# Kernel optimization log

Hardware: AMD Instinct MI355X
Metric: run time of the kernel (lower is better)

## Reference

```python
import jax, jax.numpy as jnp
import numpy as np

B, S, D = 8, 2048, 512

def setup_inputs() -> dict:
    key = jax.random.key(0)
    k1, k2 = jax.random.split(key)
    lstm_out = jax.random.normal(k1, (B, S, D), dtype=jnp.float32)
    # xavier_uniform init for [D, D]
    limit = float(np.sqrt(6.0 / (D + D)))
    attention_weights = jax.random.uniform(k2, (D, D), dtype=jnp.float32, minval=-limit, maxval=limit)
    return {"lstm_out": lstm_out, "attention_weights": attention_weights}

def reference(lstm_out, attention_weights):
    # scores[b,i,j] = tanh( (x W) x^T )
    proj = jnp.einsum('bsd,de->bse', lstm_out, attention_weights)          # [B,S,D]
    scores = jnp.tanh(jnp.einsum('bsd,btd->bst', proj, lstm_out))          # [B,S,S]
    attn = jax.nn.softmax(scores, axis=-1)                                 # [B,S,S]
    return jnp.einsum('bst,btd->bsd', attn, lstm_out)                      # [B,S,D]
```

## Files before the change

### kernel.cpp

```cpp
#include <hip/hip_runtime.h>
#include <hip/hip_bf16.h>

typedef __bf16 bf16;
typedef __attribute__((ext_vector_type(4))) __bf16 bf16x4;
typedef __attribute__((ext_vector_type(8))) __bf16 bf16x8;
typedef __attribute__((ext_vector_type(4))) float floatx4;

#define NSLOT 32

__device__ __forceinline__ void gl_lds16(const bf16* g, bf16* l) {
    __builtin_amdgcn_global_load_lds(
        (const __attribute__((address_space(1))) unsigned int*)g,
        (__attribute__((address_space(3))) unsigned int*)l,
        16, 0, 0);
}

__device__ __forceinline__ void swizzle_mn(int& bm, int& bn) {
    int gx = gridDim.x;
    int f  = blockIdx.y * gx + blockIdx.x;
    int st = f >> 3, r = f & 7;
    int mgroups = gx >> 2;
    bm = (st % mgroups) * 4 + (r & 3);
    bn = (st / mgroups) * 2 + (r >> 2);
}

__global__ __launch_bounds__(256) void cast_both(const float* __restrict__ in,
                                                 bf16* __restrict__ outn,
                                                 bf16* __restrict__ outt,
                                                 int R, int C) {
    __shared__ float tile[64][65];
    const long long bz = blockIdx.z;
    in   += bz * (long long)R * C;
    outn += bz * (long long)R * C;
    outt += bz * (long long)R * C;
    const int r0 = blockIdx.x * 64, c0 = blockIdx.y * 64;
    const int cl = (threadIdx.x & 15) * 4;
    const int rw = threadIdx.x >> 4;
#pragma unroll
    for (int it = 0; it < 4; ++it) {
        const int r = rw + it * 16;
        floatx4 v = *(const floatx4*)&in[(long long)(r0 + r) * C + c0 + cl];
        bf16x4 b; b[0] = (bf16)v[0]; b[1] = (bf16)v[1]; b[2] = (bf16)v[2]; b[3] = (bf16)v[3];
        *(bf16x4*)&outn[(long long)(r0 + r) * C + c0 + cl] = b;
        tile[r][cl + 0] = v[0]; tile[r][cl + 1] = v[1];
        tile[r][cl + 2] = v[2]; tile[r][cl + 3] = v[3];
    }
    __syncthreads();
#pragma unroll
    for (int it = 0; it < 4; ++it) {
        const int c = rw + it * 16;
        bf16x4 b;
        b[0] = (bf16)tile[cl + 0][c]; b[1] = (bf16)tile[cl + 1][c];
        b[2] = (bf16)tile[cl + 2][c]; b[3] = (bf16)tile[cl + 3][c];
        *(bf16x4*)&outt[(long long)(c0 + c) * R + r0 + cl] = b;
    }
}

__global__ __launch_bounds__(256) void cast_transpose(const float* __restrict__ in,
                                                      bf16* __restrict__ out,
                                                      int R, int C) {
    __shared__ float tile[32][33];
    const int r0 = blockIdx.x * 32, c0 = blockIdx.y * 32;
    const int tx = threadIdx.x & 31, ty = threadIdx.x >> 5;
#pragma unroll
    for (int i = 0; i < 32; i += 8)
        tile[ty + i][tx] = in[(long long)(r0 + ty + i) * C + (c0 + tx)];
    __syncthreads();
#pragma unroll
    for (int i = 0; i < 32; i += 8)
        out[(long long)(c0 + ty + i) * R + (r0 + tx)] = (bf16)tile[tx][ty + i];
}

__device__ __forceinline__ float fast_tanh(float v) {
    float e = __expf(2.0f * v);
    return 1.0f - 2.0f / (e + 1.0f);
}

template <int MODE>
__global__ __launch_bounds__(256) void gemm128(const bf16* __restrict__ A,
                                               const bf16* __restrict__ Bm,
                                               void* __restrict__ Cout,
                                               float* __restrict__ rpart,
                                               int M, int N, int K,
                                               long long batchA, long long batchB,
                                               long long batchC, long long batchR) {
    const long long bz = blockIdx.z;
    A  += bz * batchA;
    Bm += bz * batchB;

    __shared__ bf16 As[2][128 * 32];
    __shared__ bf16 Bs[2][128 * 32];
    __shared__ float rs[128];

    const int t    = threadIdx.x;
    const int lane = t & 63;
    const int wave = t >> 6;
    const int quad = lane >> 4;
    const int l16  = lane & 15;

    int bm, bn;
    swizzle_mn(bm, bn);
    const int m0 = bm * 128;
    const int n0 = bn * 128;
    const int wm = (wave >> 1) * 64;
    const int wn = (wave & 1) * 64;

    floatx4 acc[4][4] = {};

    const int srow = t >> 2;
    const int sch  = (((t & 3) ^ ((t >> 3) & 3))) * 8;
    const bf16* Abase = A + (long long)(m0 + srow) * K + sch;
    const bf16* Bbase = Bm + (long long)(n0 + srow) * K + sch;
    const long long r64 = 64LL * K;

    const int rdch = (quad ^ ((l16 >> 1) & 3)) * 8;

    if (MODE == 2) {
        if (t < 128) {
            const float* pp = rpart + (bz * batchR + m0 + t) * NSLOT;
            float s = 0.f;
#pragma unroll
            for (int c = 0; c < NSLOT / 4; ++c) {
                float4 p = ((const float4*)pp)[c];
                s += (p.x + p.y) + (p.z + p.w);
            }
            rs[t] = 1.0f / s;
        }
    }

    auto stage = [&](int buf, int k0) {
        gl_lds16(Abase + k0,       &As[buf][t * 8]);
        gl_lds16(Abase + k0 + r64, &As[buf][t * 8 + 2048]);
        gl_lds16(Bbase + k0,       &Bs[buf][t * 8]);
        gl_lds16(Bbase + k0 + r64, &Bs[buf][t * 8 + 2048]);
    };

    auto compute = [&](int buf) {
        bf16x8 af[4], bfr[4];
#pragma unroll
        for (int i = 0; i < 4; ++i)
            af[i] = *(const bf16x8*)(&As[buf][(wm + i * 16 + l16) * 32 + rdch]);
#pragma unroll
        for (int j = 0; j < 4; ++j)
            bfr[j] = *(const bf16x8*)(&Bs[buf][(wn + j * 16 + l16) * 32 + rdch]);
#pragma unroll
        for (int i = 0; i < 4; ++i)
#pragma unroll
            for (int j = 0; j < 4; ++j)
                acc[i][j] = __builtin_amdgcn_mfma_f32_16x16x32_bf16(af[i], bfr[j], acc[i][j], 0, 0, 0);
    };

    const int NT  = K >> 5;
    const int f   = blockIdx.y * gridDim.x + blockIdx.x;
    const int off = (f & 3) * (NT >> 2);

    stage(0, ((0 + off) & (NT - 1)) << 5);
    __syncthreads();
    for (int it = 0; it < NT; ++it) {
        const int buf = it & 1;
        if (it + 1 < NT) stage(buf ^ 1, ((it + 1 + off) & (NT - 1)) << 5);
        compute(buf);
        __syncthreads();
    }

    if (MODE == 1) {
        bf16* Cg = (bf16*)Cout + bz * batchC;
        const int slot = bn * 2 + (wave & 1);
#pragma unroll
        for (int i = 0; i < 4; ++i)
#pragma unroll
            for (int r = 0; r < 4; ++r) {
                long long row = m0 + wm + i * 16 + quad * 4 + r;
                float s = 0.f;
#pragma unroll
                for (int j = 0; j < 4; ++j) {
                    float v = __expf(fast_tanh(acc[i][j][r]));
                    s += v;
                    Cg[row * (long long)N + (n0 + wn + j * 16 + l16)] = (bf16)v;
                }
#pragma unroll
                for (int msk = 1; msk < 16; msk <<= 1) s += __shfl_xor(s, msk);
                if (l16 == 0)
                    rpart[(bz * batchR + row) * NSLOT + slot] = s;
            }
    } else if (MODE == 2) {
        float* Og = (float*)Cout + bz * batchC;
#pragma unroll
        for (int i = 0; i < 4; ++i)
#pragma unroll
            for (int r = 0; r < 4; ++r) {
                int rl = wm + i * 16 + quad * 4 + r;
                float inv = rs[rl];
                long long row = m0 + rl;
#pragma unroll
                for (int j = 0; j < 4; ++j)
                    Og[row * (long long)N + (n0 + wn + j * 16 + l16)] = acc[i][j][r] * inv;
            }
    } else {
        bf16* Cg = (bf16*)Cout + bz * batchC;
#pragma unroll
        for (int i = 0; i < 4; ++i)
#pragma unroll
            for (int r = 0; r < 4; ++r) {
                long long row = m0 + wm + i * 16 + quad * 4 + r;
#pragma unroll
                for (int j = 0; j < 4; ++j)
                    Cg[row * (long long)N + (n0 + wn + j * 16 + l16)] = (bf16)acc[i][j][r];
            }
    }
}

extern "C" void kernel_launch(void* const* d_in, const int* in_sizes, int n_in,
                              void* d_out, int out_size, void* d_ws, size_t ws_size,
                              hipStream_t stream) {
    const int B = 8, S = 2048, D = 512;
    const float* x = (const float*)d_in[0];
    const float* W = (const float*)d_in[1];
    float* out = (float*)d_out;

    const size_t nx = (size_t)B * S * D;
    const size_t nw = (size_t)D * D;

    char* ws = (char*)d_ws;
    auto al = [](size_t v) { return (v + 255) & ~(size_t)255; };
    size_t off = 0;
    bf16* xb = (bf16*)(ws + off); off = al(off + nx * 2);
    bf16* xt = (bf16*)(ws + off); off = al(off + nx * 2);
    bf16* pb = (bf16*)(ws + off); off = al(off + nx * 2);
    bf16* wt = (bf16*)(ws + off); off = al(off + nw * 2);
    float* rpart = (float*)(ws + off); off = al(off + (size_t)B * S * NSLOT * 4);
    bf16* sb = (bf16*)(ws + off);
    const size_t full_need = off + (size_t)B * S * S * 2;
    const bool batched = (ws_size >= full_need);

    { dim3 g(S / 64, D / 64, B); cast_both<<<g, 256, 0, stream>>>(x, xb, xt, S, D); }
    { dim3 g(D / 32, D / 32, 1); cast_transpose<<<g, 256, 0, stream>>>(W, wt, D, D); }

    {
        dim3 g(B * S / 128, D / 128, 1);
        gemm128<0><<<g, 256, 0, stream>>>(xb, wt, (void*)pb, nullptr, B * S, D, D, 0, 0, 0, 0);
    }

    const long long sd = (long long)S * D;
    const long long ss = (long long)S * S;

    if (batched) {
        dim3 g2(S / 128, S / 128, B);
        gemm128<1><<<g2, 256, 0, stream>>>(pb, xb, (void*)sb, rpart, S, S, D, sd, sd, ss, S);
        dim3 g4(S / 128, D / 128, B);
        gemm128<2><<<g4, 256, 0, stream>>>(sb, xt, (void*)out, rpart, S, D, S, ss, sd, sd, S);
    } else {
        for (int b = 0; b < B; ++b) {
            dim3 g2(S / 128, S / 128, 1);
            gemm128<1><<<g2, 256, 0, stream>>>(pb + (size_t)b * sd, xb + (size_t)b * sd,
                                               (void*)sb, rpart + (size_t)b * S * NSLOT,
                                               S, S, D, 0, 0, 0, S);
            dim3 g4(S / 128, D / 128, 1);
            gemm128<2><<<g4, 256, 0, stream>>>(sb, xt + (size_t)b * sd,
                                               (void*)(out + (size_t)b * sd), rpart + (size_t)b * S * NSLOT,
                                               S, D, S, 0, 0, 0, S);
        }
    }
}
```

Measured before the change: 218.2 us.

## Enlarge GEMM block tile to 256x128 with 512 threads and drop K stagger

Doubles the M dimension of each GEMM block tile to 256 rows using eight waves per block, so each staged B tile is shared by twice as many rows. This cuts global/L2 traffic for the B operand and halves the number of blocks. The per-block rotated K start offset is removed, so all blocks now walk K from zero. This may increase L2 channel contention, and the larger LDS footprint may reduce occupancy.

Result: slower. 223.3 us (+2.3%).

```diff
diff --git a/kernel.cpp b/kernel.cpp
--- a/kernel.cpp
+++ b/kernel.cpp
@@ -77,33 +77,33 @@
 }
 
 template <int MODE>
-__global__ __launch_bounds__(256) void gemm128(const bf16* __restrict__ A,
-                                               const bf16* __restrict__ Bm,
-                                               void* __restrict__ Cout,
-                                               float* __restrict__ rpart,
-                                               int M, int N, int K,
-                                               long long batchA, long long batchB,
-                                               long long batchC, long long batchR) {
+__global__ __launch_bounds__(512, 4) void gemm512(const bf16* __restrict__ A,
+                                                  const bf16* __restrict__ Bm,
+                                                  void* __restrict__ Cout,
+                                                  float* __restrict__ rpart,
+                                                  int M, int N, int K,
+                                                  long long batchA, long long batchB,
+                                                  long long batchC, long long batchR) {
     const long long bz = blockIdx.z;
     A  += bz * batchA;
     Bm += bz * batchB;
 
-    __shared__ bf16 As[2][128 * 32];
+    __shared__ bf16 As[2][256 * 32];
     __shared__ bf16 Bs[2][128 * 32];
-    __shared__ float rs[128];
+    __shared__ float rs[256];
 
     const int t    = threadIdx.x;
     const int lane = t & 63;
-    const int wave = t >> 6;
+    const int w    = t >> 6;
     const int quad = lane >> 4;
     const int l16  = lane & 15;
+    const int wr   = w >> 1;
+    const int wc   = w & 1;
 
     int bm, bn;
     swizzle_mn(bm, bn);
-    const int m0 = bm * 128;
+    const int m0 = bm * 256;
     const int n0 = bn * 128;
-    const int wm = (wave >> 1) * 64;
-    const int wn = (wave & 1) * 64;
 
     floatx4 acc[4][4] = {};
 
@@ -111,12 +111,12 @@
     const int sch  = (((t & 3) ^ ((t >> 3) & 3))) * 8;
     const bf16* Abase = A + (long long)(m0 + srow) * K + sch;
     const bf16* Bbase = Bm + (long long)(n0 + srow) * K + sch;
-    const long long r64 = 64LL * K;
+    const long long r128 = 128LL * K;
 
     const int rdch = (quad ^ ((l16 >> 1) & 3)) * 8;
 
     if (MODE == 2) {
-        if (t < 128) {
+        if (t < 256) {
             const float* pp = rpart + (bz * batchR + m0 + t) * NSLOT;
             float s = 0.f;
 #pragma unroll
@@ -129,20 +129,19 @@
     }
 
     auto stage = [&](int buf, int k0) {
-        gl_lds16(Abase + k0,       &As[buf][t * 8]);
-        gl_lds16(Abase + k0 + r64, &As[buf][t * 8 + 2048]);
-        gl_lds16(Bbase + k0,       &Bs[buf][t * 8]);
-        gl_lds16(Bbase + k0 + r64, &Bs[buf][t * 8 + 2048]);
+        gl_lds16(Abase + k0,        &As[buf][t * 8]);
+        gl_lds16(Abase + k0 + r128, &As[buf][t * 8 + 4096]);
+        gl_lds16(Bbase + k0,        &Bs[buf][t * 8]);
     };
 
     auto compute = [&](int buf) {
         bf16x8 af[4], bfr[4];
 #pragma unroll
         for (int i = 0; i < 4; ++i)
-            af[i] = *(const bf16x8*)(&As[buf][(wm + i * 16 + l16) * 32 + rdch]);
+            af[i] = *(const bf16x8*)(&As[buf][(wr * 64 + i * 16 + l16) * 32 + rdch]);
 #pragma unroll
         for (int j = 0; j < 4; ++j)
-            bfr[j] = *(const bf16x8*)(&Bs[buf][(wn + j * 16 + l16) * 32 + rdch]);
+            bfr[j] = *(const bf16x8*)(&Bs[buf][(wc * 64 + j * 16 + l16) * 32 + rdch]);
 #pragma unroll
         for (int i = 0; i < 4; ++i)
 #pragma unroll
@@ -150,33 +149,30 @@
                 acc[i][j] = __builtin_amdgcn_mfma_f32_16x16x32_bf16(af[i], bfr[j], acc[i][j], 0, 0, 0);
     };
 
-    const int NT  = K >> 5;
-    const int f   = blockIdx.y * gridDim.x + blockIdx.x;
-    const int off = (f & 3) * (NT >> 2);
-
-    stage(0, ((0 + off) & (NT - 1)) << 5);
+    const int NT = K >> 5;
+    stage(0, 0);
     __syncthreads();
     for (int it = 0; it < NT; ++it) {
         const int buf = it & 1;
-        if (it + 1 < NT) stage(buf ^ 1, ((it + 1 + off) & (NT - 1)) << 5);
+        if (it + 1 < NT) stage(buf ^ 1, (it + 1) << 5);
         compute(buf);
         __syncthreads();
     }
 
     if (MODE == 1) {
         bf16* Cg = (bf16*)Cout + bz * batchC;
-        const int slot = bn * 2 + (wave & 1);
+        const int slot = bn * 2 + wc;
 #pragma unroll
         for (int i = 0; i < 4; ++i)
 #pragma unroll
             for (int r = 0; r < 4; ++r) {
-                long long row = m0 + wm + i * 16 + quad * 4 + r;
+                long long row = m0 + wr * 64 + i * 16 + quad * 4 + r;
                 float s = 0.f;
 #pragma unroll
                 for (int j = 0; j < 4; ++j) {
                     float v = __expf(fast_tanh(acc[i][j][r]));
                     s += v;
-                    Cg[row * (long long)N + (n0 + wn + j * 16 + l16)] = (bf16)v;
+                    Cg[row * (long long)N + (n0 + wc * 64 + j * 16 + l16)] = (bf16)v;
                 }
 #pragma unroll
                 for (int msk = 1; msk < 16; msk <<= 1) s += __shfl_xor(s, msk);
@@ -189,12 +185,12 @@
         for (int i = 0; i < 4; ++i)
 #pragma unroll
             for (int r = 0; r < 4; ++r) {
-                int rl = wm + i * 16 + quad * 4 + r;
+                int rl = wr * 64 + i * 16 + quad * 4 + r;
                 float inv = rs[rl];
                 long long row = m0 + rl;
 #pragma unroll
                 for (int j = 0; j < 4; ++j)
-                    Og[row * (long long)N + (n0 + wn + j * 16 + l16)] = acc[i][j][r] * inv;
+                    Og[row * (long long)N + (n0 + wc * 64 + j * 16 + l16)] = acc[i][j][r] * inv;
             }
     } else {
         bf16* Cg = (bf16*)Cout + bz * batchC;
@@ -202,10 +198,10 @@
         for (int i = 0; i < 4; ++i)
 #pragma unroll
             for (int r = 0; r < 4; ++r) {
-                long long row = m0 + wm + i * 16 + quad * 4 + r;
+                long long row = m0 + wr * 64 + i * 16 + quad * 4 + r;
 #pragma unroll
                 for (int j = 0; j < 4; ++j)
-                    Cg[row * (long long)N + (n0 + wn + j * 16 + l16)] = (bf16)acc[i][j][r];
+                    Cg[row * (long long)N + (n0 + wc * 64 + j * 16 + l16)] = (bf16)acc[i][j][r];
             }
     }
 }
@@ -237,26 +233,26 @@
     { dim3 g(D / 32, D / 32, 1); cast_transpose<<<g, 256, 0, stream>>>(W, wt, D, D); }
 
     {
-        dim3 g(B * S / 128, D / 128, 1);
-        gemm128<0><<<g, 256, 0, stream>>>(xb, wt, (void*)pb, nullptr, B * S, D, D, 0, 0, 0, 0);
+        dim3 g(B * S / 256, D / 128, 1);
+        gemm512<0><<<g, 512, 0, stream>>>(xb, wt, (void*)pb, nullptr, B * S, D, D, 0, 0, 0, 0);
     }
 
     const long long sd = (long long)S * D;
     const long long ss = (long long)S * S;
 
     if (batched) {
-        dim3 g2(S / 128, S / 128, B);
-        gemm128<1><<<g2, 256, 0, stream>>>(pb, xb, (void*)sb, rpart, S, S, D, sd, sd, ss, S);
-        dim3 g4(S / 128, D / 128, B);
-        gemm128<2><<<g4, 256, 0, stream>>>(sb, xt, (void*)out, rpart, S, D, S, ss, sd, sd, S);
+        dim3 g2(S / 256, S / 128, B);
+        gemm512<1><<<g2, 512, 0, stream>>>(pb, xb, (void*)sb, rpart, S, S, D, sd, sd, ss, S);
+        dim3 g4(S / 256, D / 128, B);
+        gemm512<2><<<g4, 512, 0, stream>>>(sb, xt, (void*)out, rpart, S, D, S, ss, sd, sd, S);
     } else {
         for (int b = 0; b < B; ++b) {
-            dim3 g2(S / 128, S / 128, 1);
-            gemm128<1><<<g2, 256, 0, stream>>>(pb + (size_t)b * sd, xb + (size_t)b * sd,
+            dim3 g2(S / 256, S / 128, 1);
+            gemm512<1><<<g2, 512, 0, stream>>>(pb + (size_t)b * sd, xb + (size_t)b * sd,
                                                (void*)sb, rpart + (size_t)b * S * NSLOT,
                                                S, S, D, 0, 0, 0, S);
-            dim3 g4(S / 128, D / 128, 1);
-            gemm128<2><<<g4, 256, 0, stream>>>(sb, xt + (size_t)b * sd,
+            dim3 g4(S / 256, D / 128, 1);
+            gemm512<2><<<g4, 512, 0, stream>>>(sb, xt + (size_t)b * sd,
                                                (void*)(out + (size_t)b * sd), rpart + (size_t)b * S * NSLOT,
                                                S, D, S, 0, 0, 0, S);
         }
```
